# Optimization experiments

Measured on AMD Instinct MI355X. Metric: run time of the kernel, lower is better.

Reference implementation:

```python
import jax, jax.numpy as jnp
import numpy as np

BN_EPS = 1e-5

def _bn(x, p):
    # p rows: gamma, beta, running_mean, running_var (eval-mode BatchNorm1d)
    g, b, m, v = p[0], p[1], p[2], p[3]
    return (x - m) * jax.lax.rsqrt(v + BN_EPS) * g + b

def setup_inputs() -> dict:
    key = jax.random.key(0)
    ks = iter(jax.random.split(key, 32))
    B, P, T, E, H = 16, 64, 8, 64, 64
    batch = B * P
    def w(shape, scale=0.1):
        return (jax.random.normal(next(ks), shape, dtype=jnp.float32) * scale)
    def bn_pack(d):
        k1, k2, k3, k4 = jax.random.split(next(ks), 4)
        gamma = 1.0 + 0.1 * jax.random.normal(k1, (d,), dtype=jnp.float32)
        beta = 0.1 * jax.random.normal(k2, (d,), dtype=jnp.float32)
        mean = 0.1 * jax.random.normal(k3, (d,), dtype=jnp.float32)
        var = 0.5 + jax.random.uniform(k4, (d,), dtype=jnp.float32)
        return jnp.stack([gamma, beta, mean, var], axis=0)
    return {
        "h_states": w((1, batch, H), 1.0),
        "end_pos": w((batch, 2), 1.0),
        "vx": w((T, batch), 1.0),
        "vy": w((T, batch), 1.0),
        "agent_type": jax.random.uniform(next(ks), (T, batch, 1), dtype=jnp.float32),
        "ws_w": w((2, E)), "ws_b": w((E,)),
        "wv_w": w((2, E)), "wv_b": w((E,)),
        "wa_w": w((6, E)), "wa_b": w((E,)),
        "att1_w": w((E, 1024)), "att1_b": w((1024,)), "att_bn1": bn_pack(1024),
        "att2_w": w((1024, 1)), "att2_b": w((1,)), "att_bn2": bn_pack(1),
        "pre1_w": w((E + H, 512)), "pre1_b": w((512,)), "pre_bn1": bn_pack(512),
        "pre2_w": w((512, 1024)), "pre2_b": w((1024,)), "pre_bn2": bn_pack(1024),
        "num_ped": P,
    }

def reference(h_states, end_pos, vx, vy, agent_type,
              ws_w, ws_b, wv_w, wv_b, wa_w, wa_b,
              att1_w, att1_b, att_bn1, att2_w, att2_b, att_bn2,
              pre1_w, pre1_b, pre_bn1, pre2_w, pre2_b, pre_bn2,
              num_ped):
    P = num_ped
    batch = end_pos.shape[0]
    B = batch // P  # uniform groups (seq_start_end = [(b*P, (b+1)*P)])
    H = h_states.shape[-1]
    h = h_states.reshape(batch, H).reshape(B, P, H)            # curr_hidden per group
    pos = end_pos.reshape(B, P, 2)
    # k = i*P + j: repeated row = pos[j], 'transposed' row = pos[i]
    rel = pos[:, None, :, :] - pos[:, :, None, :]               # [B, i, j, 2]
    rel_emb = rel @ ws_w + ws_b                                 # [B, i, j, E]
    # attention_mlp: Linear->BN->ReLU->Linear->BN->ReLU (make_mlp applies BN+act after every layer)
    a1 = jax.nn.relu(_bn(rel_emb @ att1_w + att1_b, att_bn1))   # [B, i, j, 1024]
    scores = jax.nn.relu(_bn(a1 @ att2_w + att2_b, att_bn2))    # [B, i, j, 1]
    # torch.softmax(scores, dim=1) on shape (n*n, 1): softmax over a singleton -> all ones
    aw = jax.nn.softmax(scores, axis=-1)
    # velocity embedding: computed in the original then discarded (dead code, kept for fidelity)
    vel = jnp.stack([vx[-1].reshape(B, P), vy[-1].reshape(B, P)], axis=-1)
    _vel_emb = vel @ wv_w + wv_b  # noqa: F841 (unused, matches original)
    # curr_agent_type.repeat(num_ped, 6): row k=i*P+j -> type[j] tiled to 6 features
    at6 = jnp.repeat(agent_type[0].reshape(B, P, 1), 6, axis=-1)  # [B, j, 6]
    at_emb = at6 @ wa_w + wa_b                                    # [B, j, E]
    feat_j = jnp.concatenate([h, at_emb], axis=-1)                # [B, j, H+E]
    weighted = jnp.broadcast_to(feat_j[:, None, :, :], (B, P, P, feat_j.shape[-1])) * (0.05 * aw)
    p1 = jax.nn.relu(_bn(weighted @ pre1_w + pre1_b, pre_bn1))    # [B, i, j, 512]
    p2 = jax.nn.relu(_bn(p1 @ pre2_w + pre2_b, pre_bn2))          # [B, i, j, 1024]
    pool = p2.max(axis=2)                                         # view(n,n,-1).max(1): max over j
    return pool.reshape(batch, -1)
```

## Files before the change

kernel.cpp:

```cpp
#include <hip/hip_runtime.h>
#include <hip/hip_bf16.h>

#define BN_EPS 1e-5f

typedef float f32x4 __attribute__((ext_vector_type(4)));
typedef __bf16 bfx8 __attribute__((ext_vector_type(8)));
typedef __bf16 bfx4 __attribute__((ext_vector_type(4)));


__global__ __launch_bounds__(256) void k0_prep(
    const float* __restrict__ w2, const float* __restrict__ w1,
    const float* __restrict__ h, const float* __restrict__ at,
    const float* __restrict__ wa_w, const float* __restrict__ wa_b,
    const float* __restrict__ b1, const float* __restrict__ bn1,
    const float* __restrict__ b2, const float* __restrict__ bn2,
    __bf16* __restrict__ w2t, __bf16* __restrict__ w1t,
    __bf16* __restrict__ xg, float* __restrict__ scsh)
{
    const int t  = threadIdx.x;
    const int bx = blockIdx.x;

    if (bx < 144) {
        __shared__ float tile[64][69];
        int kt0, n0, src_ld, dst_ld;
        const float* src;
        __bf16* dst;
        if (bx < 128) {
            kt0 = (bx & 7) * 64;  n0 = (bx >> 3) * 64;
            src = w2; src_ld = 1024; dst = w2t; dst_ld = 512;
        } else {
            const int bt = bx - 128;
            kt0 = (bt & 1) * 64;  n0 = (bt >> 1) * 64;
            src = w1; src_ld = 512; dst = w1t; dst_ld = 128;
        }
        #pragma unroll
        for (int i = 0; i < 4; ++i) {
            const int idx = t + i * 256;
            const int kk  = idx >> 4;
            const int nq  = (idx & 15) * 4;
            const f32x4 val = *(const f32x4*)&src[(size_t)(kt0 + kk) * src_ld + n0 + nq];
            #pragma unroll
            for (int j = 0; j < 4; ++j) tile[kk][nq + j] = val[j];
        }
        __syncthreads();
        #pragma unroll
        for (int i = 0; i < 2; ++i) {
            const int idx = t + i * 256;
            const int n   = idx >> 3;
            const int kq  = (idx & 7) * 8;
            bfx8 o;
            #pragma unroll
            for (int j = 0; j < 8; ++j) o[j] = (__bf16)tile[kq + j][n];
            *(bfx8*)&dst[(size_t)(n0 + n) * dst_ld + kt0 + kq] = o;
        }
    } else if (bx < 160) {
        __shared__ float S[64];
        const int r0 = (bx - 144) * 64;
        if (t < 64) {
            float s = 0.f;
            #pragma unroll
            for (int q = 0; q < 6; ++q) s += wa_w[q * 64 + t];
            S[t] = s;
        }
        __syncthreads();
        #pragma unroll
        for (int i = 0; i < 4; ++i) {
            const int idx = t + i * 256;
            const int row = idx >> 4;
            const int cg  = (idx & 15) * 8;
            bfx8 o;
            if (cg < 64) {
                const f32x4 v0 = *(const f32x4*)&h[(size_t)(r0 + row) * 64 + cg];
                const f32x4 v1 = *(const f32x4*)&h[(size_t)(r0 + row) * 64 + cg + 4];
                #pragma unroll
                for (int j = 0; j < 4; ++j) {
                    o[j]     = (__bf16)(0.05f * v0[j]);
                    o[4 + j] = (__bf16)(0.05f * v1[j]);
                }
            } else {
                const float a = at[r0 + row];
                #pragma unroll
                for (int j = 0; j < 8; ++j) {
                    const int e = cg - 64 + j;
                    o[j] = (__bf16)(0.05f * fmaf(a, S[e], wa_b[e]));
                }
            }
            *(bfx8*)&xg[(size_t)(r0 + row) * 128 + cg] = o;
        }
    } else {
        for (int c = t; c < 512; c += 256) {
            const float s = rsqrtf(bn1[1536 + c] + BN_EPS) * bn1[c];
            scsh[c]       = s;
            scsh[512 + c] = (b1[c] - bn1[1024 + c]) * s + bn1[512 + c];
        }
        for (int c = t; c < 1024; c += 256) {
            const float s  = rsqrtf(bn2[3072 + c] + BN_EPS) * bn2[c];
            scsh[1024 + c] = s;
            scsh[2048 + c] = (b2[c] - bn2[2048 + c]) * s + bn2[1024 + c];
        }
    }
}

__global__ __launch_bounds__(512, 2) void kmain(
    const __bf16* __restrict__ xg,
    const __bf16* __restrict__ w1t,
    const __bf16* __restrict__ w2t,
    const float* __restrict__ scsh,
    float* __restrict__ out)
{
    const int cc   = blockIdx.x;
    const int b    = blockIdx.y;
    const int t    = threadIdx.x;
    const int wid  = t >> 6;
    const int lane = t & 63;
    const int l15  = lane & 15;
    const int lhi  = lane >> 4;
    const int c0w  = wid * 64;

    __shared__ __bf16 x_lds[64][136];
    __shared__ __bf16 p1_lds[64][520];
    __shared__ __bf16 B2_lds[64][520];
    __shared__ float  red[4][64];

    bfx8 xfrag[2];
    #pragma unroll
    for (int i = 0; i < 2; ++i) {
        const int idx = t + i * 512;
        const int row = idx >> 4;
        const int cg  = (idx & 15) * 8;
        xfrag[i] = *(const bfx8*)&xg[(size_t)(b * 64 + row) * 128 + cg];
    }
    bfx8 b1r[16];
    #pragma unroll
    for (int ks = 0; ks < 4; ++ks)
        #pragma unroll
        for (int cf = 0; cf < 4; ++cf)
            b1r[ks * 4 + cf] = *(const bfx8*)&w1t[
                (size_t)(c0w + cf * 16 + l15) * 128 + ks * 32 + lhi * 8];
    #pragma unroll
    for (int i = 0; i < 2; ++i) {
        const int idx = t + i * 512;
        const int row = idx >> 4;
        const int cg  = (idx & 15) * 8;
        *(bfx8*)&x_lds[row][cg] = xfrag[i];
    }
    __syncthreads();

    f32x4 b2stage[8];
    {
        const __bf16* base = w2t + (size_t)(cc * 64) * 512;
        #pragma unroll
        for (int i = 0; i < 8; ++i) {
            const int n = i * 8 + wid;
            b2stage[i] = *(const f32x4*)(base + (size_t)n * 512 + lane * 8);
        }
    }
    f32x4 sc[4], sh[4];
    #pragma unroll
    for (int cf = 0; cf < 4; ++cf) {
        const int c4 = c0w + cf * 16 + lhi * 4;
        sc[cf] = *(const f32x4*)&scsh[c4];
        sh[cf] = *(const f32x4*)&scsh[512 + c4];
    }

    f32x4 acc1[4][4] = {};
    #pragma unroll
    for (int ks = 0; ks < 4; ++ks) {
        bfx8 bf_[4];
        #pragma unroll
        for (int mf = 0; mf < 4; ++mf)
            bf_[mf] = *(const bfx8*)&x_lds[mf * 16 + l15][ks * 32 + lhi * 8];
        #pragma unroll
        for (int cf = 0; cf < 4; ++cf)
            #pragma unroll
            for (int mf = 0; mf < 4; ++mf)
                acc1[cf][mf] = __builtin_amdgcn_mfma_f32_16x16x32_bf16(
                    b1r[ks * 4 + cf], bf_[mf], acc1[cf][mf], 0, 0, 0);
    }

    #pragma unroll
    for (int i = 0; i < 8; ++i) {
        const int n = i * 8 + wid;
        *(f32x4*)((char*)&B2_lds[0][0] + (size_t)n * 1040 + lane * 16) =
            b2stage[i];
    }
    #pragma unroll
    for (int cf = 0; cf < 4; ++cf)
        #pragma unroll
        for (int mf = 0; mf < 4; ++mf) {
            bfx4 pk;
            #pragma unroll
            for (int r = 0; r < 4; ++r)
                pk[r] = (__bf16)fmaxf(
                    fmaf(acc1[cf][mf][r], sc[cf][r], sh[cf][r]), 0.f);
            *(bfx4*)&p1_lds[mf * 16 + l15][c0w + cf * 16 + lhi * 4] = pk;
        }
    __syncthreads();

    const int mrow  = (wid >> 1) * 16;
    const int nbase = (wid & 1) * 32;
    float s2[2], h2[2];
    #pragma unroll
    for (int nf = 0; nf < 2; ++nf) {
        const int ng = cc * 64 + nbase + nf * 16 + l15;
        s2[nf] = scsh[1024 + ng];
        h2[nf] = scsh[2048 + ng];
    }
    f32x4 acc2[2] = {};
    #pragma unroll
    for (int ks = 0; ks < 16; ++ks) {
        const bfx8 a = *(const bfx8*)&p1_lds[mrow + l15][ks * 32 + lhi * 8];
        #pragma unroll
        for (int nf = 0; nf < 2; ++nf) {
            const bfx8 bb =
                *(const bfx8*)&B2_lds[nbase + nf * 16 + l15][ks * 32 + lhi * 8];
            acc2[nf] = __builtin_amdgcn_mfma_f32_16x16x32_bf16(a, bb, acc2[nf], 0, 0, 0);
        }
    }

    #pragma unroll
    for (int nf = 0; nf < 2; ++nf) {
        float mm = 0.f;
        #pragma unroll
        for (int r = 0; r < 4; ++r)
            mm = fmaxf(mm, fmaxf(fmaf(acc2[nf][r], s2[nf], h2[nf]), 0.f));
        mm = fmaxf(mm, __shfl_xor(mm, 16));
        mm = fmaxf(mm, __shfl_xor(mm, 32));
        if (lane < 16) red[wid >> 1][nbase + nf * 16 + lane] = mm;
    }
    __syncthreads();

    #pragma unroll
    for (int i = 0; i < 2; ++i) {
        const int q   = t + i * 512;
        const int row = q >> 4;
        const int cq  = (q & 15) * 4;
        const f32x4 r0 = *(const f32x4*)&red[0][cq];
        const f32x4 r1 = *(const f32x4*)&red[1][cq];
        const f32x4 r2 = *(const f32x4*)&red[2][cq];
        const f32x4 r3 = *(const f32x4*)&red[3][cq];
        f32x4 pv;
        #pragma unroll
        for (int j = 0; j < 4; ++j)
            pv[j] = fmaxf(fmaxf(r0[j], r1[j]), fmaxf(r2[j], r3[j]));
        *(f32x4*)&out[(size_t)(b * 64 + row) * 1024 + cc * 64 + cq] = pv;
    }
}

extern "C" void kernel_launch(void* const* d_in, const int* in_sizes, int n_in,
                              void* d_out, int out_size, void* d_ws, size_t ws_size,
                              hipStream_t stream) {
    const float* h    = (const float*)d_in[0];
    const float* at   = (const float*)d_in[4];
    const float* wa_w = (const float*)d_in[9];
    const float* wa_b = (const float*)d_in[10];
    const float* w1   = (const float*)d_in[17];
    const float* b1   = (const float*)d_in[18];
    const float* bn1  = (const float*)d_in[19];
    const float* w2   = (const float*)d_in[20];
    const float* b2   = (const float*)d_in[21];
    const float* bn2  = (const float*)d_in[22];

    char* ws = (char*)d_ws;
    __bf16* w2t = (__bf16*)ws;
    __bf16* w1t = (__bf16*)(ws + (1 << 20));
    __bf16* xg  = (__bf16*)(ws + (1 << 20) + (128 << 10));
    float*  scsh = (float*)(ws + (1 << 20) + (384 << 10));
    float*  out  = (float*)d_out;

    k0_prep<<<161, 256, 0, stream>>>(w2, w1, h, at, wa_w, wa_b,
                                     b1, bn1, b2, bn2, w2t, w1t, xg, scsh);
    kmain<<<dim3(16, 16), 512, 0, stream>>>(xg, w1t, w2t, scsh, out);
}
```

Baseline: 19.04 us.

## Split second GEMM K across wave pairs with 32x32 per-wave tiles and LDS reduction

Each of the 8 waves now computes a 32x32 output tile over half of the K=512 reduction, instead of a 16x32 tile over the full K. This raises fragment reuse, with each A and B LDS read feeding two MFMAs instead of one or two, and shortens each wave's MFMA dependency chain. The partial sums of the two K-halves are combined through the reused x_lds buffer as scratch, which costs an extra barrier, LDS traffic, and idle waves during the epilogue.

After: 19.40 us. No clear change (+1.9%).

```diff
diff --git a/kernel.cpp b/kernel.cpp
--- a/kernel.cpp
+++ b/kernel.cpp
@@ -120,7 +120,7 @@
     __shared__ __bf16 x_lds[64][136];
     __shared__ __bf16 p1_lds[64][520];
     __shared__ __bf16 B2_lds[64][520];
-    __shared__ float  red[4][64];
+    __shared__ float  red[2][64];
 
     bfx8 xfrag[2];
     #pragma unroll
@@ -197,36 +197,70 @@
         }
     __syncthreads();
 
-    const int mrow  = (wid >> 1) * 16;
-    const int nbase = (wid & 1) * 32;
+    const int tt    = wid >> 1;
+    const int khalf = wid & 1;
+    const int tm    = (tt >> 1) * 32;
+    const int tn    = (tt & 1) * 32;
+    const int kofs  = khalf * 256;
+
     float s2[2], h2[2];
     #pragma unroll
     for (int nf = 0; nf < 2; ++nf) {
-        const int ng = cc * 64 + nbase + nf * 16 + l15;
+        const int ng = cc * 64 + tn + nf * 16 + l15;
         s2[nf] = scsh[1024 + ng];
         h2[nf] = scsh[2048 + ng];
     }
-    f32x4 acc2[2] = {};
-    #pragma unroll
-    for (int ks = 0; ks < 16; ++ks) {
-        const bfx8 a = *(const bfx8*)&p1_lds[mrow + l15][ks * 32 + lhi * 8];
+
+    f32x4 acc2[2][2] = {};
+    #pragma unroll
+    for (int ks = 0; ks < 8; ++ks) {
+        bfx8 a[2], bb[2];
+        #pragma unroll
+        for (int mf = 0; mf < 2; ++mf)
+            a[mf] = *(const bfx8*)&p1_lds[tm + mf * 16 + l15][kofs + ks * 32 + lhi * 8];
+        #pragma unroll
+        for (int nf = 0; nf < 2; ++nf)
+            bb[nf] = *(const bfx8*)&B2_lds[tn + nf * 16 + l15][kofs + ks * 32 + lhi * 8];
+        #pragma unroll
+        for (int mf = 0; mf < 2; ++mf)
+            #pragma unroll
+            for (int nf = 0; nf < 2; ++nf)
+                acc2[mf][nf] = __builtin_amdgcn_mfma_f32_16x16x32_bf16(
+                    a[mf], bb[nf], acc2[mf][nf], 0, 0, 0);
+    }
+
+    float* scratch = (float*)&x_lds[0][0];
+    if (khalf) {
+        #pragma unroll
+        for (int mf = 0; mf < 2; ++mf)
+            #pragma unroll
+            for (int nf = 0; nf < 2; ++nf)
+                *(f32x4*)&scratch[(tt * 64 + lane) * 17 + (mf * 2 + nf) * 4] =
+                    acc2[mf][nf];
+    }
+    __syncthreads();
+    if (!khalf) {
+        #pragma unroll
+        for (int mf = 0; mf < 2; ++mf)
+            #pragma unroll
+            for (int nf = 0; nf < 2; ++nf) {
+                const f32x4 p =
+                    *(const f32x4*)&scratch[(tt * 64 + lane) * 17 + (mf * 2 + nf) * 4];
+                #pragma unroll
+                for (int r = 0; r < 4; ++r) acc2[mf][nf][r] += p[r];
+            }
         #pragma unroll
         for (int nf = 0; nf < 2; ++nf) {
-            const bfx8 bb =
-                *(const bfx8*)&B2_lds[nbase + nf * 16 + l15][ks * 32 + lhi * 8];
-            acc2[nf] = __builtin_amdgcn_mfma_f32_16x16x32_bf16(a, bb, acc2[nf], 0, 0, 0);
-        }
-    }
-
-    #pragma unroll
-    for (int nf = 0; nf < 2; ++nf) {
-        float mm = 0.f;
-        #pragma unroll
-        for (int r = 0; r < 4; ++r)
-            mm = fmaxf(mm, fmaxf(fmaf(acc2[nf][r], s2[nf], h2[nf]), 0.f));
-        mm = fmaxf(mm, __shfl_xor(mm, 16));
-        mm = fmaxf(mm, __shfl_xor(mm, 32));
-        if (lane < 16) red[wid >> 1][nbase + nf * 16 + lane] = mm;
+            float mm = 0.f;
+            #pragma unroll
+            for (int mf = 0; mf < 2; ++mf)
+                #pragma unroll
+                for (int r = 0; r < 4; ++r)
+                    mm = fmaxf(mm, fmaxf(fmaf(acc2[mf][nf][r], s2[nf], h2[nf]), 0.f));
+            mm = fmaxf(mm, __shfl_xor(mm, 16));
+            mm = fmaxf(mm, __shfl_xor(mm, 32));
+            if (lane < 16) red[tm >> 5][tn + nf * 16 + lane] = mm;
+        }
     }
     __syncthreads();
 
@@ -237,12 +271,10 @@
         const int cq  = (q & 15) * 4;
         const f32x4 r0 = *(const f32x4*)&red[0][cq];
         const f32x4 r1 = *(const f32x4*)&red[1][cq];
-        const f32x4 r2 = *(const f32x4*)&red[2][cq];
-        const f32x4 r3 = *(const f32x4*)&red[3][cq];
         f32x4 pv;
         #pragma unroll
         for (int j = 0; j < 4; ++j)
-            pv[j] = fmaxf(fmaxf(r0[j], r1[j]), fmaxf(r2[j], r3[j]));
+            pv[j] = fmaxf(r0[j], r1[j]);
         *(f32x4*)&out[(size_t)(b * 64 + row) * 1024 + cc * 64 + cq] = pv;
     }
 }
```

## Fold rank-1 agent-type embedding into layer-1 epilogue, halving GEMM1 K

Applied to the files above, without the earlier changes.

The agent-type half of the layer-1 input is rank-1 in the scalar agent type. Its product with the lower half of W1 is now precomputed in the prep kernel as per-channel vectors u and v, with the BN scale folded in. The main kernel applies a*u+v in its epilogue, so GEMM1 runs over K=64 instead of 128, and xg and the w1t staging shrink. This cuts the GEMM1 work and loads that each of the 16 column blocks repeats. In exchange it adds a small reduction in the prep kernel and a per-row agent-type load in the main kernel.

Result: faster. 17.59 us (median of 2 runs) (-7.6%).

```diff
diff --git a/kernel.cpp b/kernel.cpp
--- a/kernel.cpp
+++ b/kernel.cpp
@@ -20,7 +20,7 @@
     const int t  = threadIdx.x;
     const int bx = blockIdx.x;
 
-    if (bx < 144) {
+    if (bx < 136) {
         __shared__ float tile[64][69];
         int kt0, n0, src_ld, dst_ld;
         const float* src;
@@ -29,9 +29,8 @@
             kt0 = (bx & 7) * 64;  n0 = (bx >> 3) * 64;
             src = w2; src_ld = 1024; dst = w2t; dst_ld = 512;
         } else {
-            const int bt = bx - 128;
-            kt0 = (bt & 1) * 64;  n0 = (bt >> 1) * 64;
-            src = w1; src_ld = 512; dst = w1t; dst_ld = 128;
+            kt0 = 0;  n0 = (bx - 128) * 64;
+            src = w1; src_ld = 512; dst = w1t; dst_ld = 64;
         }
         #pragma unroll
         for (int i = 0; i < 4; ++i) {
@@ -53,50 +52,63 @@
             for (int j = 0; j < 8; ++j) o[j] = (__bf16)tile[kq + j][n];
             *(bfx8*)&dst[(size_t)(n0 + n) * dst_ld + kt0 + kq] = o;
         }
+    } else if (bx < 152) {
+        const int r0 = (bx - 136) * 64;
+        #pragma unroll
+        for (int i = 0; i < 2; ++i) {
+            const int idx = t + i * 256;
+            const int row = idx >> 3;
+            const int cg  = (idx & 7) * 8;
+            const f32x4 v0 = *(const f32x4*)&h[(size_t)(r0 + row) * 64 + cg];
+            const f32x4 v1 = *(const f32x4*)&h[(size_t)(r0 + row) * 64 + cg + 4];
+            bfx8 o;
+            #pragma unroll
+            for (int j = 0; j < 4; ++j) {
+                o[j]     = (__bf16)(0.05f * v0[j]);
+                o[4 + j] = (__bf16)(0.05f * v1[j]);
+            }
+            *(bfx8*)&xg[(size_t)(r0 + row) * 64 + cg] = o;
+        }
     } else if (bx < 160) {
-        __shared__ float S[64];
-        const int r0 = (bx - 144) * 64;
+        __shared__ float Sl[64], Wbl[64];
+        __shared__ float pu[4][64], pv[4][64];
+        const int c0 = (bx - 152) * 64;
         if (t < 64) {
             float s = 0.f;
             #pragma unroll
             for (int q = 0; q < 6; ++q) s += wa_w[q * 64 + t];
-            S[t] = s;
+            Sl[t]  = 0.05f * s;
+            Wbl[t] = 0.05f * wa_b[t];
         }
         __syncthreads();
+        const int cl   = t & 63;
+        const int eseg = t >> 6;
+        float su = 0.f, sv = 0.f;
+        for (int e = eseg * 16; e < eseg * 16 + 16; ++e) {
+            const float w = w1[(size_t)(64 + e) * 512 + c0 + cl];
+            su = fmaf(Sl[e], w, su);
+            sv = fmaf(Wbl[e], w, sv);
+        }
+        pu[eseg][cl] = su;
+        pv[eseg][cl] = sv;
+        __syncthreads();
+        if (t < 64) {
+            const int c = c0 + t;
+            const float u = pu[0][t] + pu[1][t] + pu[2][t] + pu[3][t];
+            const float v = pv[0][t] + pv[1][t] + pv[2][t] + pv[3][t];
+            const float s = rsqrtf(bn1[1536 + c] + BN_EPS) * bn1[c];
+            const float base = (b1[c] - bn1[1024 + c]) * s + bn1[512 + c];
+            scsh[c]        = s;
+            scsh[512 + c]  = u * s;
+            scsh[1024 + c] = v * s + base;
+        }
+    } else {
         #pragma unroll
         for (int i = 0; i < 4; ++i) {
-            const int idx = t + i * 256;
-            const int row = idx >> 4;
-            const int cg  = (idx & 15) * 8;
-            bfx8 o;
-            if (cg < 64) {
-                const f32x4 v0 = *(const f32x4*)&h[(size_t)(r0 + row) * 64 + cg];
-                const f32x4 v1 = *(const f32x4*)&h[(size_t)(r0 + row) * 64 + cg + 4];
-                #pragma unroll
-                for (int j = 0; j < 4; ++j) {
-                    o[j]     = (__bf16)(0.05f * v0[j]);
-                    o[4 + j] = (__bf16)(0.05f * v1[j]);
-                }
-            } else {
-                const float a = at[r0 + row];
-                #pragma unroll
-                for (int j = 0; j < 8; ++j) {
-                    const int e = cg - 64 + j;
-                    o[j] = (__bf16)(0.05f * fmaf(a, S[e], wa_b[e]));
-                }
-            }
-            *(bfx8*)&xg[(size_t)(r0 + row) * 128 + cg] = o;
-        }
-    } else {
-        for (int c = t; c < 512; c += 256) {
-            const float s = rsqrtf(bn1[1536 + c] + BN_EPS) * bn1[c];
-            scsh[c]       = s;
-            scsh[512 + c] = (b1[c] - bn1[1024 + c]) * s + bn1[512 + c];
-        }
-        for (int c = t; c < 1024; c += 256) {
+            const int c = t + i * 256;
             const float s  = rsqrtf(bn2[3072 + c] + BN_EPS) * bn2[c];
-            scsh[1024 + c] = s;
-            scsh[2048 + c] = (b2[c] - bn2[2048 + c]) * s + bn2[1024 + c];
+            scsh[1536 + c] = s;
+            scsh[2560 + c] = (b2[c] - bn2[2048 + c]) * s + bn2[1024 + c];
         }
     }
 }
@@ -105,6 +117,7 @@
     const __bf16* __restrict__ xg,
     const __bf16* __restrict__ w1t,
     const __bf16* __restrict__ w2t,
+    const float* __restrict__ at,
     const float* __restrict__ scsh,
     float* __restrict__ out)
 {
@@ -117,32 +130,28 @@
     const int lhi  = lane >> 4;
     const int c0w  = wid * 64;
 
-    __shared__ __bf16 x_lds[64][136];
+    __shared__ __bf16 x_lds[64][72];
     __shared__ __bf16 p1_lds[64][520];
     __shared__ __bf16 B2_lds[64][520];
     __shared__ float  red[4][64];
 
-    bfx8 xfrag[2];
-    #pragma unroll
-    for (int i = 0; i < 2; ++i) {
-        const int idx = t + i * 512;
-        const int row = idx >> 4;
-        const int cg  = (idx & 15) * 8;
-        xfrag[i] = *(const bfx8*)&xg[(size_t)(b * 64 + row) * 128 + cg];
-    }
-    bfx8 b1r[16];
-    #pragma unroll
-    for (int ks = 0; ks < 4; ++ks)
+    bfx8 xfrag;
+    {
+        const int row = t >> 3;
+        const int cg  = (t & 7) * 8;
+        xfrag = *(const bfx8*)&xg[(size_t)(b * 64 + row) * 64 + cg];
+    }
+    bfx8 b1r[8];
+    #pragma unroll
+    for (int ks = 0; ks < 2; ++ks)
         #pragma unroll
         for (int cf = 0; cf < 4; ++cf)
             b1r[ks * 4 + cf] = *(const bfx8*)&w1t[
-                (size_t)(c0w + cf * 16 + l15) * 128 + ks * 32 + lhi * 8];
-    #pragma unroll
-    for (int i = 0; i < 2; ++i) {
-        const int idx = t + i * 512;
-        const int row = idx >> 4;
-        const int cg  = (idx & 15) * 8;
-        *(bfx8*)&x_lds[row][cg] = xfrag[i];
+                (size_t)(c0w + cf * 16 + l15) * 64 + ks * 32 + lhi * 8];
+    {
+        const int row = t >> 3;
+        const int cg  = (t & 7) * 8;
+        *(bfx8*)&x_lds[row][cg] = xfrag;
     }
     __syncthreads();
 
@@ -155,17 +164,21 @@
             b2stage[i] = *(const f32x4*)(base + (size_t)n * 512 + lane * 8);
         }
     }
-    f32x4 sc[4], sh[4];
+    float at4[4];
+    #pragma unroll
+    for (int mf = 0; mf < 4; ++mf) at4[mf] = at[b * 64 + mf * 16 + l15];
+    f32x4 sc[4], us[4], vs[4];
     #pragma unroll
     for (int cf = 0; cf < 4; ++cf) {
         const int c4 = c0w + cf * 16 + lhi * 4;
         sc[cf] = *(const f32x4*)&scsh[c4];
-        sh[cf] = *(const f32x4*)&scsh[512 + c4];
+        us[cf] = *(const f32x4*)&scsh[512 + c4];
+        vs[cf] = *(const f32x4*)&scsh[1024 + c4];
     }
 
     f32x4 acc1[4][4] = {};
     #pragma unroll
-    for (int ks = 0; ks < 4; ++ks) {
+    for (int ks = 0; ks < 2; ++ks) {
         bfx8 bf_[4];
         #pragma unroll
         for (int mf = 0; mf < 4; ++mf)
@@ -190,9 +203,11 @@
         for (int mf = 0; mf < 4; ++mf) {
             bfx4 pk;
             #pragma unroll
-            for (int r = 0; r < 4; ++r)
+            for (int r = 0; r < 4; ++r) {
+                const float base = fmaf(at4[mf], us[cf][r], vs[cf][r]);
                 pk[r] = (__bf16)fmaxf(
-                    fmaf(acc1[cf][mf][r], sc[cf][r], sh[cf][r]), 0.f);
+                    fmaf(acc1[cf][mf][r], sc[cf][r], base), 0.f);
+            }
             *(bfx4*)&p1_lds[mf * 16 + l15][c0w + cf * 16 + lhi * 4] = pk;
         }
     __syncthreads();
@@ -203,8 +218,8 @@
     #pragma unroll
     for (int nf = 0; nf < 2; ++nf) {
         const int ng = cc * 64 + nbase + nf * 16 + l15;
-        s2[nf] = scsh[1024 + ng];
-        h2[nf] = scsh[2048 + ng];
+        s2[nf] = scsh[1536 + ng];
+        h2[nf] = scsh[2560 + ng];
     }
     f32x4 acc2[2] = {};
     #pragma unroll
@@ -262,13 +277,13 @@
     const float* bn2  = (const float*)d_in[22];
 
     char* ws = (char*)d_ws;
-    __bf16* w2t = (__bf16*)ws;
-    __bf16* w1t = (__bf16*)(ws + (1 << 20));
-    __bf16* xg  = (__bf16*)(ws + (1 << 20) + (128 << 10));
-    float*  scsh = (float*)(ws + (1 << 20) + (384 << 10));
+    __bf16* w2t  = (__bf16*)ws;
+    __bf16* w1t  = (__bf16*)(ws + (1 << 20));
+    __bf16* xg   = (__bf16*)(ws + (1 << 20) + (64 << 10));
+    float*  scsh = (float*)(ws + (1 << 20) + (192 << 10));
     float*  out  = (float*)d_out;
 
     k0_prep<<<161, 256, 0, stream>>>(w2, w1, h, at, wa_w, wa_b,
                                      b1, bn1, b2, bn2, w2t, w1t, xg, scsh);
-    kmain<<<dim3(16, 16), 512, 0, stream>>>(xg, w1t, w2t, scsh, out);
+    kmain<<<dim3(16, 16), 512, 0, stream>>>(xg, w1t, w2t, at, scsh, out);
 }
```
